# Performance work log

Measured on AMD Instinct MI355X. Metric: run time of the kernel, lower is better.

Reference implementation:

```python
import jax, jax.numpy as jnp
import numpy as np

N_NODES = 40000
N_EDGES = 640000
D_FEAT = 128


def setup_inputs() -> dict:
    key = jax.random.key(0)
    k1, k2, k3, k4 = jax.random.split(key, 4)
    rows = jax.random.randint(k1, (N_EDGES,), 0, N_NODES, dtype=jnp.int32)
    cols = jax.random.randint(k2, (N_EDGES,), 0, N_NODES, dtype=jnp.int32)
    vals = jax.random.uniform(k3, (N_EDGES,), dtype=jnp.float32)
    annotations = jax.random.normal(k4, (N_NODES, D_FEAT), dtype=jnp.float32)
    return {"rows": rows, "cols": cols, "vals": vals, "annotations": annotations}


def reference(rows, cols, vals, annotations):
    # out = adjacent @ annotations, with adjacent given in COO form:
    # adjacent[rows[e], cols[e]] = vals[e].
    # SpMM as gather -> scale -> segment_sum over destination rows.
    gathered = annotations[cols] * vals[:, None]          # [E, d]
    out = jax.ops.segment_sum(gathered, rows, num_segments=N_NODES)  # [N, d]
    return out
```

## Files before the change

### kernel.cpp

```cpp
#include <hip/hip_runtime.h>


constexpr int N_NODES = 40000;
constexpr int N_EDGES = 640000;
constexpr int D_FEAT  = 128;
constexpr int CAP     = 32;
constexpr int OVF_CAP = 16384;

constexpr size_t WS_CURSOR = 0;
constexpr size_t WS_OVFCNT = 160000;
constexpr size_t WS_OVF    = 160256;
constexpr size_t WS_ANNB   = 422400;
constexpr size_t WS_PAIRS  = 10662400;
constexpr size_t WS_NEEDED = 20902400;

typedef int   v2i __attribute__((ext_vector_type(2)));
typedef float v2f __attribute__((ext_vector_type(2)));
typedef int   v4i __attribute__((ext_vector_type(4)));
typedef float v4f __attribute__((ext_vector_type(4)));

__device__ __forceinline__ unsigned f2b_rne(float f) {
    unsigned b = __float_as_uint(f);
    return (b + 0x7fffu + ((b >> 16) & 1u)) >> 16;
}

__global__ __launch_bounds__(256) void convert_kernel(
    const float* __restrict__ ann, uint2* __restrict__ annb,
    int* __restrict__ cursor, int* __restrict__ ovfcnt)
{
    int t = blockIdx.x * blockDim.x + threadIdx.x;
    if (t < N_NODES) cursor[t] = 0;
    if (t == 0) *ovfcnt = 0;
    if (t < N_NODES * D_FEAT / 4) {
        v4f f = __builtin_nontemporal_load(reinterpret_cast<const v4f*>(ann) + t);
        uint2 o;
        o.x = f2b_rne(f.x) | (f2b_rne(f.y) << 16);
        o.y = f2b_rne(f.z) | (f2b_rne(f.w) << 16);
        annb[t] = o;
    }
}

__device__ __forceinline__ void scatter_one(
    int r, int c, float v, int* cursor, v2i* pairs,
    int* ovfcnt, int4* ovf)
{
    int slot = atomicAdd(&cursor[r], 1);
    if (slot < CAP) {
        v2i p;
        p.x = c;
        p.y = __float_as_int(v);
        __builtin_nontemporal_store(p, pairs + (r * CAP + slot));
    } else {
        int o = atomicAdd(ovfcnt, 1);
        if (o < OVF_CAP) ovf[o] = make_int4(r, c, __float_as_int(v), 0);
    }
}

__global__ __launch_bounds__(256) void scatter_kernel(
    const int*   __restrict__ rows,
    const int*   __restrict__ cols,
    const float* __restrict__ vals,
    int* __restrict__ cursor, v2i* __restrict__ pairs,
    int* __restrict__ ovfcnt, int4* __restrict__ ovf)
{
    int t = blockIdx.x * blockDim.x + threadIdx.x;
    if (t < N_EDGES / 4) {
        v4i r4 = __builtin_nontemporal_load(reinterpret_cast<const v4i*>(rows) + t);
        v4i c4 = __builtin_nontemporal_load(reinterpret_cast<const v4i*>(cols) + t);
        v4f v4 = __builtin_nontemporal_load(reinterpret_cast<const v4f*>(vals) + t);
        scatter_one(r4.x, c4.x, v4.x, cursor, pairs, ovfcnt, ovf);
        scatter_one(r4.y, c4.y, v4.y, cursor, pairs, ovfcnt, ovf);
        scatter_one(r4.z, c4.z, v4.z, cursor, pairs, ovfcnt, ovf);
        scatter_one(r4.w, c4.w, v4.w, cursor, pairs, ovfcnt, ovf);
    }
}

__global__ __launch_bounds__(256) void pull_kernel(
    const unsigned* __restrict__ annb,
    const int*      __restrict__ cursor,
    const v2i*      __restrict__ pairs,
    const int*      __restrict__ ovfcnt,
    const int4*     __restrict__ ovf,
    float*          __restrict__ out)
{
    int r    = (blockIdx.x * blockDim.x + threadIdx.x) >> 6;
    int lane = threadIdx.x & 63;
    if (r >= N_NODES) return;

    int cntr = cursor[r];
    int cnt  = cntr > CAP ? CAP : cntr;

    int2 pr = make_int2(0, 0);
    if (lane < cnt) {
        v2i p = __builtin_nontemporal_load(pairs + (r * CAP + lane));
        pr.x = p.x;
        pr.y = p.y;
    }

    float2 acc = make_float2(0.f, 0.f);
    int nb = (cnt + 7) & ~7;
    for (int j = 0; j < nb; j += 8) {
        #pragma unroll
        for (int k = 0; k < 8; k++) {
            int      c = __shfl(pr.x, j + k, 64);
            float    v = __int_as_float(__shfl(pr.y, j + k, 64));
            unsigned p = annb[c * (D_FEAT / 2) + lane];
            float a0 = __uint_as_float(p << 16);
            float a1 = __uint_as_float(p & 0xffff0000u);
            acc.x += v * a0;
            acc.y += v * a1;
        }
    }

    if (cntr > CAP) {
        int n = *ovfcnt;
        n = n > OVF_CAP ? OVF_CAP : n;
        for (int i = 0; i < n; i++) {
            int4 e = ovf[i];
            if (e.x == r) {
                unsigned p = annb[e.y * (D_FEAT / 2) + lane];
                float    v = __int_as_float(e.z);
                acc.x += v * __uint_as_float(p << 16);
                acc.y += v * __uint_as_float(p & 0xffff0000u);
            }
        }
    }

    v2f o;
    o.x = acc.x;
    o.y = acc.y;
    __builtin_nontemporal_store(
        o, reinterpret_cast<v2f*>(out) + ((size_t)r * (D_FEAT / 2) + lane));
}

__global__ __launch_bounds__(256) void spmm_scatter_kernel(
    const int*   __restrict__ rows,
    const int*   __restrict__ cols,
    const float* __restrict__ vals,
    const float* __restrict__ ann,
    float*       __restrict__ out)
{
    int t = blockIdx.x * blockDim.x + threadIdx.x;
    int e = t >> 5;
    if (e >= N_EDGES) return;
    int lane = t & 31;
    int   r = rows[e];
    int   c = cols[e];
    float v = vals[e];
    float4 a = reinterpret_cast<const float4*>(ann)[(size_t)c * (D_FEAT / 4) + lane];
    float* o = out + (size_t)r * D_FEAT + lane * 4;
    unsafeAtomicAdd(o + 0, v * a.x);
    unsafeAtomicAdd(o + 1, v * a.y);
    unsafeAtomicAdd(o + 2, v * a.z);
    unsafeAtomicAdd(o + 3, v * a.w);
}

extern "C" void kernel_launch(void* const* d_in, const int* in_sizes, int n_in,
                              void* d_out, int out_size, void* d_ws, size_t ws_size,
                              hipStream_t stream) {
    const int*   rows = (const int*)  d_in[0];
    const int*   cols = (const int*)  d_in[1];
    const float* vals = (const float*)d_in[2];
    const float* ann  = (const float*)d_in[3];
    float*       out  = (float*)      d_out;

    if (ws_size < WS_NEEDED) {
        hipMemsetAsync(out, 0, (size_t)out_size * sizeof(float), stream);
        const long long total_threads = (long long)N_EDGES * 32;
        spmm_scatter_kernel<<<dim3((unsigned)((total_threads + 255) / 256)),
                              dim3(256), 0, stream>>>(rows, cols, vals, ann, out);
        return;
    }

    char*     ws     = (char*)d_ws;
    int*      cursor = (int*)     (ws + WS_CURSOR);
    int*      ovfcnt = (int*)     (ws + WS_OVFCNT);
    int4*     ovf    = (int4*)    (ws + WS_OVF);
    unsigned* annb   = (unsigned*)(ws + WS_ANNB);
    v2i*      pairs  = (v2i*)     (ws + WS_PAIRS);

    convert_kernel<<<dim3((N_NODES * D_FEAT / 4 + 255) / 256), dim3(256), 0, stream>>>(
        ann, (uint2*)annb, cursor, ovfcnt);

    scatter_kernel<<<dim3((N_EDGES / 4 + 255) / 256), dim3(256), 0, stream>>>(
        rows, cols, vals, cursor, pairs, ovfcnt, ovf);

    const long long pull_threads = (long long)N_NODES * 64;
    pull_kernel<<<dim3((unsigned)((pull_threads + 255) / 256)), dim3(256), 0, stream>>>(
        annb, cursor, pairs, ovfcnt, ovf, out);
}
```

Baseline: 149.1 us.

## Merge scatter and convert kernels, pad cursors, and split pull gathers into column passes

Combines the edge-scatter and bf16 conversion into one launch split by block index, and zeroes the cursors and overflow counter with a memset instead of inside the convert kernel. Pads each row cursor to 16 ints so atomics on different rows do not share a cache line. The pull kernel now makes four passes over each row's edges and in each pass only gathers source rows in one quarter of the node range, aiming to keep the concurrently gathered working set cache-resident. The cost is repeated shuffles and divergent branches per pass, a larger cursor array to clear, and scatter now using one edge per thread.

```diff
diff --git a/kernel.cpp b/kernel.cpp
--- a/kernel.cpp
+++ b/kernel.cpp
@@ -6,72 +6,65 @@
 constexpr int D_FEAT  = 128;
 constexpr int CAP     = 32;
 constexpr int OVF_CAP = 16384;
+constexpr int CSTR    = 16;
+constexpr int NPASS   = 4;
+constexpr int PASS_W  = N_NODES / NPASS;
 
 constexpr size_t WS_CURSOR = 0;
-constexpr size_t WS_OVFCNT = 160000;
-constexpr size_t WS_OVF    = 160256;
-constexpr size_t WS_ANNB   = 422400;
-constexpr size_t WS_PAIRS  = 10662400;
-constexpr size_t WS_NEEDED = 20902400;
+constexpr size_t WS_OVFCNT = 2560000;
+constexpr size_t WS_OVF    = 2560256;
+constexpr size_t WS_ANNB   = 2822400;
+constexpr size_t WS_PAIRS  = 13062400;
+constexpr size_t WS_ZERO   = 2560256;
+constexpr size_t WS_NEEDED = 23302400;
 
-typedef int   v2i __attribute__((ext_vector_type(2)));
-typedef float v2f __attribute__((ext_vector_type(2)));
-typedef int   v4i __attribute__((ext_vector_type(4)));
-typedef float v4f __attribute__((ext_vector_type(4)));
+constexpr int SCAT_BLOCKS = N_EDGES / 256;
+constexpr int CONV_BLOCKS = (N_NODES * D_FEAT / 8) / 256;
+
+typedef int      v2i __attribute__((ext_vector_type(2)));
+typedef float    v2f __attribute__((ext_vector_type(2)));
+typedef float    v4f __attribute__((ext_vector_type(4)));
+typedef unsigned v4u __attribute__((ext_vector_type(4)));
 
 __device__ __forceinline__ unsigned f2b_rne(float f) {
     unsigned b = __float_as_uint(f);
     return (b + 0x7fffu + ((b >> 16) & 1u)) >> 16;
 }
 
-__global__ __launch_bounds__(256) void convert_kernel(
-    const float* __restrict__ ann, uint2* __restrict__ annb,
-    int* __restrict__ cursor, int* __restrict__ ovfcnt)
-{
-    int t = blockIdx.x * blockDim.x + threadIdx.x;
-    if (t < N_NODES) cursor[t] = 0;
-    if (t == 0) *ovfcnt = 0;
-    if (t < N_NODES * D_FEAT / 4) {
-        v4f f = __builtin_nontemporal_load(reinterpret_cast<const v4f*>(ann) + t);
-        uint2 o;
-        o.x = f2b_rne(f.x) | (f2b_rne(f.y) << 16);
-        o.y = f2b_rne(f.z) | (f2b_rne(f.w) << 16);
-        annb[t] = o;
-    }
-}
-
-__device__ __forceinline__ void scatter_one(
-    int r, int c, float v, int* cursor, v2i* pairs,
-    int* ovfcnt, int4* ovf)
-{
-    int slot = atomicAdd(&cursor[r], 1);
-    if (slot < CAP) {
-        v2i p;
-        p.x = c;
-        p.y = __float_as_int(v);
-        __builtin_nontemporal_store(p, pairs + (r * CAP + slot));
-    } else {
-        int o = atomicAdd(ovfcnt, 1);
-        if (o < OVF_CAP) ovf[o] = make_int4(r, c, __float_as_int(v), 0);
-    }
-}
-
-__global__ __launch_bounds__(256) void scatter_kernel(
+__global__ __launch_bounds__(256) void build_kernel(
     const int*   __restrict__ rows,
     const int*   __restrict__ cols,
     const float* __restrict__ vals,
+    const float* __restrict__ ann,
+    unsigned*    __restrict__ annb,
     int* __restrict__ cursor, v2i* __restrict__ pairs,
     int* __restrict__ ovfcnt, int4* __restrict__ ovf)
 {
-    int t = blockIdx.x * blockDim.x + threadIdx.x;
-    if (t < N_EDGES / 4) {
-        v4i r4 = __builtin_nontemporal_load(reinterpret_cast<const v4i*>(rows) + t);
-        v4i c4 = __builtin_nontemporal_load(reinterpret_cast<const v4i*>(cols) + t);
-        v4f v4 = __builtin_nontemporal_load(reinterpret_cast<const v4f*>(vals) + t);
-        scatter_one(r4.x, c4.x, v4.x, cursor, pairs, ovfcnt, ovf);
-        scatter_one(r4.y, c4.y, v4.y, cursor, pairs, ovfcnt, ovf);
-        scatter_one(r4.z, c4.z, v4.z, cursor, pairs, ovfcnt, ovf);
-        scatter_one(r4.w, c4.w, v4.w, cursor, pairs, ovfcnt, ovf);
+    if (blockIdx.x < SCAT_BLOCKS) {
+        int e = blockIdx.x * 256 + threadIdx.x;
+        int   r = __builtin_nontemporal_load(rows + e);
+        int   c = __builtin_nontemporal_load(cols + e);
+        float v = __builtin_nontemporal_load(vals + e);
+        int slot = atomicAdd(&cursor[r * CSTR], 1);
+        if (slot < CAP) {
+            v2i p;
+            p.x = c;
+            p.y = __float_as_int(v);
+            pairs[r * CAP + slot] = p;
+        } else {
+            int o = atomicAdd(ovfcnt, 1);
+            if (o < OVF_CAP) ovf[o] = make_int4(r, c, __float_as_int(v), 0);
+        }
+    } else {
+        int t = (blockIdx.x - SCAT_BLOCKS) * 256 + threadIdx.x;
+        v4f f0 = __builtin_nontemporal_load(reinterpret_cast<const v4f*>(ann) + 2 * t);
+        v4f f1 = __builtin_nontemporal_load(reinterpret_cast<const v4f*>(ann) + 2 * t + 1);
+        v4u o;
+        o.x = f2b_rne(f0.x) | (f2b_rne(f0.y) << 16);
+        o.y = f2b_rne(f0.z) | (f2b_rne(f0.w) << 16);
+        o.z = f2b_rne(f1.x) | (f2b_rne(f1.y) << 16);
+        o.w = f2b_rne(f1.z) | (f2b_rne(f1.w) << 16);
+        reinterpret_cast<v4u*>(annb)[t] = o;
     }
 }
 
@@ -85,9 +78,8 @@
 {
     int r    = (blockIdx.x * blockDim.x + threadIdx.x) >> 6;
     int lane = threadIdx.x & 63;
-    if (r >= N_NODES) return;
 
-    int cntr = cursor[r];
+    int cntr = cursor[r * CSTR];
     int cnt  = cntr > CAP ? CAP : cntr;
 
     int2 pr = make_int2(0, 0);
@@ -99,16 +91,20 @@
 
     float2 acc = make_float2(0.f, 0.f);
     int nb = (cnt + 7) & ~7;
-    for (int j = 0; j < nb; j += 8) {
-        #pragma unroll
-        for (int k = 0; k < 8; k++) {
-            int      c = __shfl(pr.x, j + k, 64);
-            float    v = __int_as_float(__shfl(pr.y, j + k, 64));
-            unsigned p = annb[c * (D_FEAT / 2) + lane];
-            float a0 = __uint_as_float(p << 16);
-            float a1 = __uint_as_float(p & 0xffff0000u);
-            acc.x += v * a0;
-            acc.y += v * a1;
+    for (int pass = 0; pass < NPASS; pass++) {
+        int lo = pass * PASS_W;
+        int hi = lo + PASS_W;
+        for (int j = 0; j < nb; j += 8) {
+            #pragma unroll
+            for (int k = 0; k < 8; k++) {
+                int c = __shfl(pr.x, j + k, 64);
+                if (c >= lo && c < hi) {
+                    float    v = __int_as_float(__shfl(pr.y, j + k, 64));
+                    unsigned p = annb[c * (D_FEAT / 2) + lane];
+                    acc.x += v * __uint_as_float(p << 16);
+                    acc.y += v * __uint_as_float(p & 0xffff0000u);
+                }
+            }
         }
     }
 
@@ -179,11 +175,10 @@
     unsigned* annb   = (unsigned*)(ws + WS_ANNB);
     v2i*      pairs  = (v2i*)     (ws + WS_PAIRS);
 
-    convert_kernel<<<dim3((N_NODES * D_FEAT / 4 + 255) / 256), dim3(256), 0, stream>>>(
-        ann, (uint2*)annb, cursor, ovfcnt);
+    hipMemsetAsync(cursor, 0, WS_ZERO, stream);
 
-    scatter_kernel<<<dim3((N_EDGES / 4 + 255) / 256), dim3(256), 0, stream>>>(
-        rows, cols, vals, cursor, pairs, ovfcnt, ovf);
+    build_kernel<<<dim3(SCAT_BLOCKS + CONV_BLOCKS), dim3(256), 0, stream>>>(
+        rows, cols, vals, ann, annb, cursor, pairs, ovfcnt, ovf);
 
     const long long pull_threads = (long long)N_NODES * 64;
     pull_kernel<<<dim3((unsigned)((pull_threads + 255) / 256)), dim3(256), 0, stream>>>(
```

Result: slower. 190.3 us (+27.6%).
